# Kernel tuning notes

Hardware: AMD Instinct MI355X
Metric: run time of the kernel (lower is better)

The kernel has to match this reference:

```python
import jax, jax.numpy as jnp
import numpy as np

N = 50000
F_IN = 256
F_OUT = 256
K = 5
E = 1_600_000
SQRT_2PI = float(np.sqrt(2.0 * np.pi))
SQRT_2 = float(np.sqrt(2.0))


def _ex_relu(mu, sigma):
    # expected value of relu(Normal(mu, sigma)) with sigma = variance
    is_zero = sigma == 0
    safe_sigma = jnp.where(is_zero, 1e-10, sigma)
    sqrt_sigma = jnp.sqrt(safe_sigma)
    w = mu / sqrt_sigma
    nr = sqrt_sigma * (jnp.exp(-0.5 * w * w) / SQRT_2PI
                       + 0.5 * w * (1.0 + jax.lax.erf(w / SQRT_2)))
    return jnp.where(is_zero, jnp.maximum(mu, 0.0), nr)


def _conv(h, src, dst):
    # SimpleConv(aggr='add', combine_root='self_loop'):
    # out[d] = h[d] + sum_{(s,d) in edges} h[s];  h: [K, N, O]
    agg = jnp.zeros_like(h).at[:, dst, :].add(h[:, src, :])
    return h + agg


def setup_inputs() -> dict:
    key = jax.random.key(0)
    ks = jax.random.split(key, 7)
    x = jax.random.normal(ks[0], (N, F_IN), dtype=jnp.float32)
    edges = jax.random.randint(ks[1], (2, E), 0, N, dtype=jnp.int64)
    mask = jax.random.randint(ks[2], (N, F_IN), 0, 2) == 1  # True = missing
    logp = jax.random.normal(ks[3], (K,), dtype=jnp.float32)
    means = jax.random.normal(ks[4], (K, F_IN), dtype=jnp.float32)
    logvars = jax.random.normal(ks[5], (K, F_IN), dtype=jnp.float32)
    weight = jax.random.normal(ks[6], (F_IN, F_OUT), dtype=jnp.float32) * (1.414 / np.sqrt(F_IN + F_OUT) * np.sqrt(6.0))
    bias = jnp.zeros((F_OUT,), dtype=jnp.float32)
    return {"x": x, "edges": edges, "mask": mask, "logp": logp,
            "means": means, "logvars": logvars, "weight": weight, "bias": bias}


def reference(x, edges, mask, logp, means, logvars, weight, bias):
    src, dst = edges[0], edges[1]
    variances = jnp.exp(logvars)                                   # [K, F]
    m = mask[None, :, :]                                           # [1, N, F]
    mean_mat = jnp.where(m, means[:, None, :], x[None, :, :])      # [K, N, F]
    var_mat = jnp.where(m, variances[:, None, :], 0.0)             # [K, N, F]

    transform_x = jnp.einsum('knf,fo->kno', mean_mat, weight) + bias
    transform_covs = jnp.einsum('knf,fo->kno', var_mat, weight * weight)

    conv_x = _conv(transform_x, src, dst)                          # [K, N, O]
    conv_covs = _conv(transform_covs, src, dst)                    # [K, N, O]

    expected_x = _ex_relu(conv_x, conv_covs)                       # [K, N, O]

    # GMM responsibilities over components
    diff2 = (mean_mat - means[:, None, :]) ** 2 / variances[:, None, :]
    log_n = (-0.5 * jnp.sum(diff2, axis=2)
             - 0.5 * F_IN * np.log(2.0 * np.pi)
             - 0.5 * jnp.sum(logvars))                             # [K, N]
    gamma = jax.nn.softmax(logp[:, None] + log_n, axis=0)          # [K, N]

    return jnp.sum(expected_x * gamma[:, :, None], axis=0)         # [N, O]
```

## Files before the change

kernel.cpp:

```cpp
#include <hip/hip_runtime.h>
#include <math.h>

#define F 256
#define KMIX 5
#define RECB 640
#define GR 16
#define GS 3136

typedef __attribute__((ext_vector_type(8))) short bf16x8;
typedef __attribute__((ext_vector_type(4))) float f32x4;

__device__ __forceinline__ float bf2f(unsigned short u) {
  union { unsigned int i; float f; } v; v.i = ((unsigned int)u) << 16; return v.f;
}
__device__ __forceinline__ unsigned short f2bf(float f) {
  union { float f; unsigned int i; } v; v.f = f;
  unsigned int u = v.i;
  unsigned int r = (u + 0x7fffu + ((u >> 16) & 1u)) >> 16;
  return (unsigned short)r;
}

__device__ __forceinline__ f32x4 MFMA(bf16x8 a, bf16x8 b, f32x4 c) {
  return __builtin_amdgcn_mfma_f32_16x16x32_bf16(a, b, c, 0, 0, 0);
}

__device__ __forceinline__ float ex_relu_fast(float mu, float sig) {
  const float c1 = 1.2732395447f;
  const float c2 = 2.5464790895f;
  float t = mu * mu;
  float u = t + c1 * sig;
  float v = t + c2 * sig + 1e-20f;
  float r = __builtin_amdgcn_rsqf(v);
  return 0.5f * mu + 0.5f * u * r;
}

__global__ void kzero(unsigned int* p, long long n) {
  long long i = (long long)blockIdx.x * blockDim.x + threadIdx.x;
  long long stride = (long long)gridDim.x * blockDim.x;
  for (; i < n; i += stride) p[i] = 0u;
}

__global__ __launch_bounds__(256) void k_tab(const float* __restrict__ logvars,
                                             float* __restrict__ ivar) {
  int i = blockIdx.x * 256 + threadIdx.x;
  if (i < KMIX * F) ivar[i] = __expf(-logvars[i]);
}

__global__ __launch_bounds__(256) void k_prep(
    const float* __restrict__ x, const int* __restrict__ mask,
    const float* __restrict__ logp, const float* __restrict__ means,
    const float* __restrict__ ivar,
    unsigned char* __restrict__ rec, float* __restrict__ gamma, int Npad) {
  int n = blockIdx.x;
  int f = threadIdx.x;
  int idx = n * F + f;
  float xv = x[idx];
  int m = mask[idx];
  unsigned char* rn = rec + (size_t)n * RECB;
  ((unsigned short*)rn)[f] = m ? (unsigned short)0 : f2bf(xv);
  int wave = threadIdx.x >> 6;
  int lane = threadIdx.x & 63;
  unsigned long long bal = __ballot(m != 0);
  if (lane == 0) *(unsigned long long*)(rn + 512 + wave * 8) = bal;
  float cb[KMIX];
#pragma unroll
  for (int k = 0; k < KMIX; ++k) {
    float d = xv - means[k * F + f];
    cb[k] = m ? 0.0f : d * d * ivar[k * F + f];
  }
  __shared__ float red[KMIX][4];
#pragma unroll
  for (int k = 0; k < KMIX; ++k) {
    float c = cb[k];
    for (int off = 32; off > 0; off >>= 1) c += __shfl_down(c, off, 64);
    if (lane == 0) red[k][wave] = c;
  }
  __syncthreads();
  if (threadIdx.x == 0) {
    float lg[KMIX], mx = -1e30f;
#pragma unroll
    for (int k = 0; k < KMIX; ++k) {
      float tot = red[k][0] + red[k][1] + red[k][2] + red[k][3];
      lg[k] = logp[k] - 0.5f * tot;
      mx = fmaxf(mx, lg[k]);
    }
    float den = 0.0f, e[KMIX];
#pragma unroll
    for (int k = 0; k < KMIX; ++k) { e[k] = __expf(lg[k] - mx); den += e[k]; }
    float inv = 1.0f / den;
#pragma unroll
    for (int k = 0; k < KMIX; ++k) gamma[k * Npad + n] = e[k] * inv;
  }
}

__global__ void k_count(const int* __restrict__ edges, int* __restrict__ cnt, int E) {
  int i = blockIdx.x * blockDim.x + threadIdx.x;
  if (i < E) {
    int dst = edges[E + i];
    int g = edges[i] / GS;
    atomicAdd(&cnt[dst * GR + g], 1);
  }
}

__global__ __launch_bounds__(1024) void k_scanA(const int* __restrict__ cnt,
                                                int* __restrict__ excl,
                                                int* __restrict__ bsum, int n) {
  __shared__ int s[1024];
  int t = threadIdx.x;
  int i = blockIdx.x * 1024 + t;
  int v = (i < n) ? cnt[i] : 0;
  s[t] = v;
  __syncthreads();
  for (int off = 1; off < 1024; off <<= 1) {
    int u = (t >= off) ? s[t - off] : 0;
    __syncthreads();
    s[t] += u;
    __syncthreads();
  }
  if (i < n) excl[i] = s[t] - v;
  if (t == 1023) bsum[blockIdx.x] = s[1023];
}

__global__ __launch_bounds__(1024) void k_scanB(int* __restrict__ bsum, int nb) {
  __shared__ int s[1024];
  int t = threadIdx.x;
  int v = (t < nb) ? bsum[t] : 0;
  s[t] = v;
  __syncthreads();
  for (int off = 1; off < 1024; off <<= 1) {
    int u = (t >= off) ? s[t - off] : 0;
    __syncthreads();
    s[t] += u;
    __syncthreads();
  }
  if (t < nb) bsum[t] = s[t] - v;
}

__global__ __launch_bounds__(1024) void k_scanC(int* __restrict__ offs,
                                                int* __restrict__ cur,
                                                const int* __restrict__ bsum,
                                                int n, int E) {
  int i = blockIdx.x * 1024 + threadIdx.x;
  if (i < n) {
    int v = offs[i] + bsum[blockIdx.x];
    offs[i] = v;
    cur[i] = v;
  }
  if (i == 0) offs[n] = E;
}

__global__ void k_fill(const int* __restrict__ edges, int* __restrict__ cur,
                       int* __restrict__ srclist, int E) {
  int i = blockIdx.x * blockDim.x + threadIdx.x;
  if (i < E) {
    int src = edges[i];
    int dst = edges[E + i];
    int g = src / GS;
    int pos = atomicAdd(&cur[dst * GR + g], 1);
    srclist[pos] = src;
  }
}

__global__ __launch_bounds__(1024) void k_gather(
    const unsigned char* __restrict__ rec,
    const int* __restrict__ offs, const int* __restrict__ srclist,
    unsigned short* __restrict__ xs_pack, unsigned short* __restrict__ sm_pack,
    float* __restrict__ degp1) {
  __shared__ float xs_l[16][257];
  __shared__ float sm_l[16][257];
  int tile = blockIdx.x;
  int wave = threadIdx.x >> 6, lane = threadIdx.x & 63;
  int fb = lane * 4;
  int n = tile * 16 + wave;
  const unsigned char* rn = rec + (size_t)n * RECB;
  ushort4 xv = *(const ushort4*)(rn + lane * 8);
  unsigned int mw = *(const unsigned int*)(rn + 512 + ((lane >> 3) << 2));
  unsigned int nib = (mw >> ((lane & 7) * 4)) & 0xFu;
  unsigned int macc = (nib | (nib << 7) | (nib << 14) | (nib << 21)) & 0x01010101u;
  float a0 = bf2f(xv.x), a1 = bf2f(xv.y), a2 = bf2f(xv.z), a3 = bf2f(xv.w);
  int s0 = offs[n * GR], s1 = offs[n * GR + GR];
  int i = s0;
  int nsa = 0, nsb = 0, nsc = 0, nsd = 0;
  if (i + 4 <= s1) {
    nsa = srclist[i]; nsb = srclist[i + 1]; nsc = srclist[i + 2]; nsd = srclist[i + 3];
  }
  while (i + 4 <= s1) {
    int sa = nsa, sb = nsb, sc = nsc, sd = nsd;
    const unsigned char* ra = rec + (size_t)sa * RECB;
    const unsigned char* rb = rec + (size_t)sb * RECB;
    const unsigned char* rc = rec + (size_t)sc * RECB;
    const unsigned char* rd = rec + (size_t)sd * RECB;
    ushort4 va = *(const ushort4*)(ra + lane * 8);
    ushort4 vb = *(const ushort4*)(rb + lane * 8);
    ushort4 vc = *(const ushort4*)(rc + lane * 8);
    ushort4 vd = *(const ushort4*)(rd + lane * 8);
    unsigned int wa = *(const unsigned int*)(ra + 512 + ((lane >> 3) << 2));
    unsigned int wb = *(const unsigned int*)(rb + 512 + ((lane >> 3) << 2));
    unsigned int wc = *(const unsigned int*)(rc + 512 + ((lane >> 3) << 2));
    unsigned int wd = *(const unsigned int*)(rd + 512 + ((lane >> 3) << 2));
    i += 4;
    if (i + 4 <= s1) {
      nsa = srclist[i]; nsb = srclist[i + 1]; nsc = srclist[i + 2]; nsd = srclist[i + 3];
    }
    a0 += bf2f(va.x) + bf2f(vb.x) + bf2f(vc.x) + bf2f(vd.x);
    a1 += bf2f(va.y) + bf2f(vb.y) + bf2f(vc.y) + bf2f(vd.y);
    a2 += bf2f(va.z) + bf2f(vb.z) + bf2f(vc.z) + bf2f(vd.z);
    a3 += bf2f(va.w) + bf2f(vb.w) + bf2f(vc.w) + bf2f(vd.w);
    unsigned int na = (wa >> ((lane & 7) * 4)) & 0xFu;
    unsigned int nb = (wb >> ((lane & 7) * 4)) & 0xFu;
    unsigned int nc = (wc >> ((lane & 7) * 4)) & 0xFu;
    unsigned int nd = (wd >> ((lane & 7) * 4)) & 0xFu;
    macc += (na | (na << 7) | (na << 14) | (na << 21)) & 0x01010101u;
    macc += (nb | (nb << 7) | (nb << 14) | (nb << 21)) & 0x01010101u;
    macc += (nc | (nc << 7) | (nc << 14) | (nc << 21)) & 0x01010101u;
    macc += (nd | (nd << 7) | (nd << 14) | (nd << 21)) & 0x01010101u;
  }
  for (; i < s1; ++i) {
    int s = srclist[i];
    const unsigned char* rs = rec + (size_t)s * RECB;
    ushort4 sv = *(const ushort4*)(rs + lane * 8);
    unsigned int ws = *(const unsigned int*)(rs + 512 + ((lane >> 3) << 2));
    a0 += bf2f(sv.x); a1 += bf2f(sv.y); a2 += bf2f(sv.z); a3 += bf2f(sv.w);
    unsigned int ns = (ws >> ((lane & 7) * 4)) & 0xFu;
    macc += (ns | (ns << 7) | (ns << 14) | (ns << 21)) & 0x01010101u;
  }
  xs_l[wave][fb] = a0; xs_l[wave][fb + 1] = a1; xs_l[wave][fb + 2] = a2; xs_l[wave][fb + 3] = a3;
  sm_l[wave][fb] = (float)(macc & 0xFFu);
  sm_l[wave][fb + 1] = (float)((macc >> 8) & 0xFFu);
  sm_l[wave][fb + 2] = (float)((macc >> 16) & 0xFFu);
  sm_l[wave][fb + 3] = (float)(macc >> 24);
  if (lane == 0) degp1[n] = (float)(s1 - s0 + 1);
  __syncthreads();
  if (threadIdx.x < 512) {
    int slot = threadIdx.x;
    int kt = slot >> 6, l = slot & 63;
    int r = l & 15, q = l >> 4;
    int fbase = kt * 32 + q * 8;
    bf16x8 vx, vs;
#pragma unroll
    for (int j = 0; j < 8; ++j) {
      vx[j] = (short)f2bf(xs_l[r][fbase + j]);
      vs[j] = (short)f2bf(sm_l[r][fbase + j]);
    }
    long long po = ((long long)tile * 8 + kt) * 64 + l;
    ((bf16x8*)xs_pack)[po] = vx;
    ((bf16x8*)sm_pack)[po] = vs;
  }
}

__global__ __launch_bounds__(64) void k_bpack(
    const float* __restrict__ weight, const float* __restrict__ means,
    const float* __restrict__ logvars, unsigned short* __restrict__ bpack) {
  int bid = blockIdx.x;
  int kt = bid & 7, ot = (bid >> 3) & 15, m = bid >> 7;
  int l = threadIdx.x;
  int r = l & 15, q = l >> 4;
  int o = ot * 16 + r;
  bf16x8 v;
#pragma unroll
  for (int j = 0; j < 8; ++j) {
    int f = kt * 32 + q * 8 + j;
    float wv = weight[f * F + o];
    float val;
    if (m == 0) val = wv;
    else if (m <= 5) val = means[(m - 1) * F + f] * wv;
    else val = __expf(logvars[(m - 6) * F + f]) * wv * wv;
    v[j] = (short)f2bf(val);
  }
  ((bf16x8*)bpack)[((long long)(m * 16 + ot) * 8 + kt) * 64 + l] = v;
}

__global__ __launch_bounds__(256, 3) void k_gemm(
    const unsigned short* __restrict__ xs_pack, const unsigned short* __restrict__ sm_pack,
    const unsigned short* __restrict__ bpack, const float* __restrict__ degp1,
    const float* __restrict__ gamma, const float* __restrict__ bias,
    float* __restrict__ out, int N, int Npad, int RB) {
  int L = blockIdx.x;
  int rb = (L >> 5) * 8 + (L & 7);
  int bo = (L >> 3) & 3;
  if (rb >= RB) return;
  __shared__ unsigned char sp_lds[32768];
  int tid = threadIdx.x;
  int wave = tid >> 6, lane = tid & 63;
  int rw = wave >> 1, cw = wave & 1;
  int q = lane >> 4, r16 = lane & 15;
  int rt0 = rb * 4 + rw * 2;
  int ct0 = bo * 4 + cw * 2;
  const bf16x8* XP = (const bf16x8*)xs_pack;
  const bf16x8* BP = (const bf16x8*)bpack;

  {
    const uint4* src = (const uint4*)((const unsigned char*)sm_pack + (size_t)rb * 32768) + tid;
    uint4* dst = (uint4*)(void*)sp_lds + tid;
#pragma unroll
    for (int it = 0; it < 8; ++it) dst[it * 256] = src[it * 256];
  }

  f32x4 C1[2][2];
#pragma unroll
  for (int rt = 0; rt < 2; ++rt)
#pragma unroll
    for (int cc = 0; cc < 2; ++cc) C1[rt][cc] = (f32x4){0.f, 0.f, 0.f, 0.f};
#pragma unroll
  for (int kt = 0; kt < 8; ++kt) {
    bf16x8 a0 = XP[((size_t)rt0 * 8 + kt) * 64 + lane];
    bf16x8 a1 = XP[((size_t)(rt0 + 1) * 8 + kt) * 64 + lane];
#pragma unroll
    for (int cc = 0; cc < 2; ++cc) {
      bf16x8 b = BP[((size_t)(ct0 + cc) * 8 + kt) * 64 + lane];
      C1[0][cc] = MFMA(a0, b, C1[0][cc]);
      C1[1][cc] = MFMA(a1, b, C1[1][cc]);
    }
  }

  int row0 = rb * 64 + rw * 32 + q * 4;
  {
    float dp[2][4];
#pragma unroll
    for (int rt = 0; rt < 2; ++rt)
#pragma unroll
      for (int rr = 0; rr < 4; ++rr) dp[rt][rr] = degp1[row0 + rt * 16 + rr];
    float bs[2];
#pragma unroll
    for (int cc = 0; cc < 2; ++cc) bs[cc] = bias[bo * 64 + cw * 32 + cc * 16 + r16];
#pragma unroll
    for (int rt = 0; rt < 2; ++rt)
#pragma unroll
      for (int cc = 0; cc < 2; ++cc)
#pragma unroll
        for (int rr = 0; rr < 4; ++rr) C1[rt][cc][rr] += dp[rt][rr] * bs[cc];
  }

  f32x4 outa[2][2];
#pragma unroll
  for (int rt = 0; rt < 2; ++rt)
#pragma unroll
    for (int cc = 0; cc < 2; ++cc) outa[rt][cc] = (f32x4){0.f, 0.f, 0.f, 0.f};

  __syncthreads();
  const unsigned char* myl = sp_lds + rw * 16384;

  for (int k = 0; k < KMIX; ++k) {
    float gm[2][4];
#pragma unroll
    for (int rt = 0; rt < 2; ++rt)
#pragma unroll
      for (int rr = 0; rr < 4; ++rr) gm[rt][rr] = gamma[k * Npad + row0 + rt * 16 + rr];
    f32x4 ax[2][2], ac[2][2];
#pragma unroll
    for (int rt = 0; rt < 2; ++rt)
#pragma unroll
      for (int cc = 0; cc < 2; ++cc) {
        ax[rt][cc] = C1[rt][cc];
        ac[rt][cc] = (f32x4){0.f, 0.f, 0.f, 0.f};
      }
#pragma unroll
    for (int kt = 0; kt < 8; ++kt) {
      bf16x8 sp0 = *(const bf16x8*)(myl + kt * 1024 + lane * 16);
      bf16x8 sp1 = *(const bf16x8*)(myl + 8192 + kt * 1024 + lane * 16);
#pragma unroll
      for (int cc = 0; cc < 2; ++cc) {
        int c = ct0 + cc;
        bf16x8 bw = BP[(((size_t)(1 + k) * 16 + c) * 8 + kt) * 64 + lane];
        bf16x8 bv = BP[(((size_t)(6 + k) * 16 + c) * 8 + kt) * 64 + lane];
        ax[0][cc] = MFMA(sp0, bw, ax[0][cc]);
        ax[1][cc] = MFMA(sp1, bw, ax[1][cc]);
        ac[0][cc] = MFMA(sp0, bv, ac[0][cc]);
        ac[1][cc] = MFMA(sp1, bv, ac[1][cc]);
      }
    }
#pragma unroll
    for (int rt = 0; rt < 2; ++rt)
#pragma unroll
      for (int cc = 0; cc < 2; ++cc)
#pragma unroll
        for (int rr = 0; rr < 4; ++rr) {
          float e = ex_relu_fast(ax[rt][cc][rr], ac[rt][cc][rr]);
          outa[rt][cc][rr] += gm[rt][rr] * e;
        }
  }

#pragma unroll
  for (int rt = 0; rt < 2; ++rt)
#pragma unroll
    for (int cc = 0; cc < 2; ++cc) {
      int col = bo * 64 + cw * 32 + cc * 16 + r16;
#pragma unroll
      for (int rr = 0; rr < 4; ++rr) {
        int row = row0 + rt * 16 + rr;
        if (row < N) out[(long long)row * F + col] = outa[rt][cc][rr];
      }
    }
}

extern "C" void kernel_launch(void* const* d_in, const int* in_sizes, int n_in,
                              void* d_out, int out_size, void* d_ws, size_t ws_size,
                              hipStream_t stream) {
  const float* x = (const float*)d_in[0];
  const int* edges = (const int*)d_in[1];
  const int* mask = (const int*)d_in[2];
  const float* logp = (const float*)d_in[3];
  const float* means = (const float*)d_in[4];
  const float* logvars = (const float*)d_in[5];
  const float* weight = (const float*)d_in[6];
  const float* bias = (const float*)d_in[7];
  float* out = (float*)d_out;

  int N = in_sizes[0] / F;
  int E = in_sizes[1] / 2;
  int Npad = ((N + 127) / 128) * 128;
  int RB = Npad / 64;
  int NB = N * GR;
  int SB = (NB + 1023) / 1024;

  char* w = (char*)d_ws;
  auto alloc = [&](size_t bytes) {
    char* p = w;
    w += (bytes + 255) & ~(size_t)255;
    return p;
  };
  unsigned char* rec = (unsigned char*)alloc((size_t)N * RECB);
  unsigned short* xsp = (unsigned short*)alloc((size_t)Npad * F * 2);
  unsigned short* smp = (unsigned short*)alloc((size_t)Npad * F * 2);
  unsigned short* bpk = (unsigned short*)alloc((size_t)11 * F * F * 2);
  int* cnt = (int*)alloc((size_t)NB * 4);
  int* offs = (int*)alloc((size_t)(NB + 1) * 4);
  int* cur = (int*)alloc((size_t)NB * 4);
  int* bsum = (int*)alloc((size_t)1024 * 4);
  int* srclist = (int*)alloc((size_t)E * 4);
  float* degp1 = (float*)alloc((size_t)Npad * 4);
  float* gamma = (float*)alloc((size_t)KMIX * Npad * 4);
  float* ivar = (float*)alloc((size_t)KMIX * F * 4);

  kzero<<<782, 256, 0, stream>>>((unsigned int*)cnt, NB);
  k_tab<<<(KMIX * F + 255) / 256, 256, 0, stream>>>(logvars, ivar);
  k_prep<<<N, 256, 0, stream>>>(x, mask, logp, means, ivar, rec, gamma, Npad);
  k_count<<<(E + 255) / 256, 256, 0, stream>>>(edges, cnt, E);
  k_scanA<<<SB, 1024, 0, stream>>>(cnt, offs, bsum, NB);
  k_scanB<<<1, 1024, 0, stream>>>(bsum, SB);
  k_scanC<<<SB, 1024, 0, stream>>>(offs, cur, bsum, NB, E);
  k_fill<<<(E + 255) / 256, 256, 0, stream>>>(edges, cur, srclist, E);
  k_gather<<<N / 16, 1024, 0, stream>>>(rec, offs, srclist, xsp, smp, degp1);
  k_bpack<<<11 * 16 * 8, 64, 0, stream>>>(weight, means, logvars, bpk);
  int NGG = (RB + 7) / 8;
  k_gemm<<<NGG * 32, 256, 0, stream>>>(xsp, smp, bpk, degp1, gamma, bias, out, N, Npad, RB);
}
```

Before: 762.4 us.

## Widen gather unroll to 8, interleave mean/var weight packs, unroll mixture loop

The neighbor-gather loop now loads 8 source indices and their 8 records at once instead of a 4-wide software-pipelined loop, so more independent memory requests are in flight per wave. The weight-pack kernel now stores the mean-weighted and variance-weighted B tiles interleaved, so the GEMM reads bw and bv from adjacent 16-byte slots (one 32-byte contiguous region per lane). The mixture-component loop is fully unrolled. Together these aim to raise memory-level parallelism and cut address arithmetic, at the cost of higher register pressure under the 3-blocks-per-CU launch bound.

```diff
diff --git a/kernel.cpp b/kernel.cpp
--- a/kernel.cpp
+++ b/kernel.cpp
@@ -180,40 +180,24 @@
   float a0 = bf2f(xv.x), a1 = bf2f(xv.y), a2 = bf2f(xv.z), a3 = bf2f(xv.w);
   int s0 = offs[n * GR], s1 = offs[n * GR + GR];
   int i = s0;
-  int nsa = 0, nsb = 0, nsc = 0, nsd = 0;
-  if (i + 4 <= s1) {
-    nsa = srclist[i]; nsb = srclist[i + 1]; nsc = srclist[i + 2]; nsd = srclist[i + 3];
-  }
-  while (i + 4 <= s1) {
-    int sa = nsa, sb = nsb, sc = nsc, sd = nsd;
-    const unsigned char* ra = rec + (size_t)sa * RECB;
-    const unsigned char* rb = rec + (size_t)sb * RECB;
-    const unsigned char* rc = rec + (size_t)sc * RECB;
-    const unsigned char* rd = rec + (size_t)sd * RECB;
-    ushort4 va = *(const ushort4*)(ra + lane * 8);
-    ushort4 vb = *(const ushort4*)(rb + lane * 8);
-    ushort4 vc = *(const ushort4*)(rc + lane * 8);
-    ushort4 vd = *(const ushort4*)(rd + lane * 8);
-    unsigned int wa = *(const unsigned int*)(ra + 512 + ((lane >> 3) << 2));
-    unsigned int wb = *(const unsigned int*)(rb + 512 + ((lane >> 3) << 2));
-    unsigned int wc = *(const unsigned int*)(rc + 512 + ((lane >> 3) << 2));
-    unsigned int wd = *(const unsigned int*)(rd + 512 + ((lane >> 3) << 2));
-    i += 4;
-    if (i + 4 <= s1) {
-      nsa = srclist[i]; nsb = srclist[i + 1]; nsc = srclist[i + 2]; nsd = srclist[i + 3];
-    }
-    a0 += bf2f(va.x) + bf2f(vb.x) + bf2f(vc.x) + bf2f(vd.x);
-    a1 += bf2f(va.y) + bf2f(vb.y) + bf2f(vc.y) + bf2f(vd.y);
-    a2 += bf2f(va.z) + bf2f(vb.z) + bf2f(vc.z) + bf2f(vd.z);
-    a3 += bf2f(va.w) + bf2f(vb.w) + bf2f(vc.w) + bf2f(vd.w);
-    unsigned int na = (wa >> ((lane & 7) * 4)) & 0xFu;
-    unsigned int nb = (wb >> ((lane & 7) * 4)) & 0xFu;
-    unsigned int nc = (wc >> ((lane & 7) * 4)) & 0xFu;
-    unsigned int nd = (wd >> ((lane & 7) * 4)) & 0xFu;
-    macc += (na | (na << 7) | (na << 14) | (na << 21)) & 0x01010101u;
-    macc += (nb | (nb << 7) | (nb << 14) | (nb << 21)) & 0x01010101u;
-    macc += (nc | (nc << 7) | (nc << 14) | (nc << 21)) & 0x01010101u;
-    macc += (nd | (nd << 7) | (nd << 14) | (nd << 21)) & 0x01010101u;
+  for (; i + 8 <= s1; i += 8) {
+    int sx[8];
+#pragma unroll
+    for (int j = 0; j < 8; ++j) sx[j] = srclist[i + j];
+    ushort4 vv[8];
+    unsigned int ww[8];
+#pragma unroll
+    for (int j = 0; j < 8; ++j) {
+      const unsigned char* rj = rec + (size_t)sx[j] * RECB;
+      vv[j] = *(const ushort4*)(rj + lane * 8);
+      ww[j] = *(const unsigned int*)(rj + 512 + ((lane >> 3) << 2));
+    }
+#pragma unroll
+    for (int j = 0; j < 8; ++j) {
+      a0 += bf2f(vv[j].x); a1 += bf2f(vv[j].y); a2 += bf2f(vv[j].z); a3 += bf2f(vv[j].w);
+      unsigned int nj = (ww[j] >> ((lane & 7) * 4)) & 0xFu;
+      macc += (nj | (nj << 7) | (nj << 14) | (nj << 21)) & 0x01010101u;
+    }
   }
   for (; i < s1; ++i) {
     int s = srclist[i];
@@ -267,7 +251,15 @@
     else val = __expf(logvars[(m - 6) * F + f]) * wv * wv;
     v[j] = (short)f2bf(val);
   }
-  ((bf16x8*)bpack)[((long long)(m * 16 + ot) * 8 + kt) * 64 + l] = v;
+  size_t idx;
+  if (m == 0) {
+    idx = ((size_t)ot * 8 + kt) * 64 + l;
+  } else {
+    int s = (m <= 5) ? 0 : 1;
+    int k = (m <= 5) ? (m - 1) : (m - 6);
+    idx = 8192 + ((((size_t)k * 16 + ot) * 8 + kt) * 64 + l) * 2 + s;
+  }
+  ((bf16x8*)bpack)[idx] = v;
 }
 
 __global__ __launch_bounds__(256, 3) void k_gemm(
@@ -288,6 +280,7 @@
   int ct0 = bo * 4 + cw * 2;
   const bf16x8* XP = (const bf16x8*)xs_pack;
   const bf16x8* BP = (const bf16x8*)bpack;
+  const bf16x8* BPp = BP + 8192;
 
   {
     const uint4* src = (const uint4*)((const unsigned char*)sm_pack + (size_t)rb * 32768) + tid;
@@ -340,6 +333,7 @@
   __syncthreads();
   const unsigned char* myl = sp_lds + rw * 16384;
 
+#pragma unroll
   for (int k = 0; k < KMIX; ++k) {
     float gm[2][4];
 #pragma unroll
@@ -361,8 +355,9 @@
 #pragma unroll
       for (int cc = 0; cc < 2; ++cc) {
         int c = ct0 + cc;
-        bf16x8 bw = BP[(((size_t)(1 + k) * 16 + c) * 8 + kt) * 64 + lane];
-        bf16x8 bv = BP[(((size_t)(6 + k) * 16 + c) * 8 + kt) * 64 + lane];
+        const bf16x8* pp = &BPp[((((size_t)k * 16 + c) * 8 + kt) * 64 + lane) * 2];
+        bf16x8 bw = pp[0];
+        bf16x8 bv = pp[1];
         ax[0][cc] = MFMA(sp0, bw, ax[0][cc]);
         ax[1][cc] = MFMA(sp1, bw, ax[1][cc]);
         ac[0][cc] = MFMA(sp0, bv, ac[0][cc]);
```

After: 989.5 us. +29.8%, slower.
